# Kernel optimization log

Hardware: AMD Instinct MI355X
Metric: run time of the kernel (lower is better)

The kernel has to match this reference:

```python
import jax, jax.numpy as jnp
import numpy as np

N = 50000        # nodes
E = 1_600_000    # edges (avg degree 32)
D_IN = 128
HID = 256
D_OUT = 128      # must equal D_IN for the residual add


def setup_inputs() -> dict:
    key = jax.random.key(0)
    k0, k1, k2, k3 = jax.random.split(key, 4)
    x = jax.random.normal(k0, (N, D_IN), dtype=jnp.float32)
    edge_index = jax.random.randint(k1, (2, E), 0, N, dtype=jnp.int32)
    # GCNConv params (lin: Linear without bias in PyG, plus additive bias)
    W1 = jax.random.normal(k2, (D_IN, HID), dtype=jnp.float32) / np.sqrt(D_IN)
    b1 = jnp.zeros((HID,), jnp.float32)
    W2 = jax.random.normal(k3, (HID, D_OUT), dtype=jnp.float32) / np.sqrt(HID)
    b2 = jnp.zeros((D_OUT,), jnp.float32)
    return {"x": x, "edge_index": edge_index, "W1": W1, "b1": b1, "W2": W2, "b2": b2}


def _gcn_conv(x, src, dst, norm, W, b, n):
    # PyG GCNConv: transform, gather source features, scale by sym-norm, scatter-add to dst.
    h = x @ W                        # [n, d_out]
    msg = h[src] * norm[:, None]     # [E+n, d_out] gathered messages
    out = jax.ops.segment_sum(msg, dst, num_segments=n)
    return out + b


def reference(x, edge_index, W1, b1, W2, b2):
    n = x.shape[0]
    # add self loops (GCNConv default add_self_loops=True)
    loops = jnp.arange(n, dtype=edge_index.dtype)
    src = jnp.concatenate([edge_index[0], loops])
    dst = jnp.concatenate([edge_index[1], loops])
    # symmetric normalization D^{-1/2} (A+I) D^{-1/2}
    deg = jax.ops.segment_sum(jnp.ones_like(dst, dtype=x.dtype), dst, num_segments=n)
    dinv = jnp.where(deg > 0, jax.lax.rsqrt(deg), 0.0)
    norm = dinv[src] * dinv[dst]
    skip = x  # nn.Identity skip connection
    h = jax.nn.relu(_gcn_conv(x, src, dst, norm, W1, b1, n))
    out = _gcn_conv(h, src, dst, norm, W2, b2, n)
    # classification_layer treated as identity; original .double() cast kept in fp32
    return out + skip
```

## Files before the change

kernel.cpp:

```cpp
#include <hip/hip_runtime.h>

#define D_IN 128
#define HID 256
#define BKT_SHIFT 9
#define BKT_SIZE 512
#define CHUNK 4096
#define PAD_SLACK 4096
#define LSTR 264

typedef __attribute__((ext_vector_type(8))) short short8;
typedef __attribute__((ext_vector_type(4))) float floatx4;

static __device__ __forceinline__ unsigned short f2b(float f) {
  unsigned u = __float_as_uint(f);
  unsigned r = (u + 0x7fffu + ((u >> 16) & 1u)) >> 16;
  return (unsigned short)r;
}

static __device__ __forceinline__ void unpack8(uint4 v, float* f) {
  f[0] = __uint_as_float(v.x << 16); f[1] = __uint_as_float(v.x & 0xffff0000u);
  f[2] = __uint_as_float(v.y << 16); f[3] = __uint_as_float(v.y & 0xffff0000u);
  f[4] = __uint_as_float(v.z << 16); f[5] = __uint_as_float(v.z & 0xffff0000u);
  f[6] = __uint_as_float(v.w << 16); f[7] = __uint_as_float(v.w & 0xffff0000u);
}

static __device__ __forceinline__ void acc_fma(float* acc, uint4 v, float w) {
  float g[8];
  unpack8(v, g);
#pragma unroll
  for (int d = 0; d < 8; ++d) acc[d] = fmaf(g[d], w, acc[d]);
}


__global__ __launch_bounds__(256) void bin_hist_kernel(const int* __restrict__ dst,
                                                       int* __restrict__ bkt_cnt,
                                                       int E, int nbkt) {
  __shared__ int hist[128];
  const int tid = threadIdx.x;
  if (tid < nbkt) hist[tid] = 0;
  __syncthreads();
  const int base = blockIdx.x * CHUNK;
  const int end = min(base + CHUNK, E);
  for (int e = base + tid; e < end; e += 256)
    atomicAdd(&hist[dst[e] >> BKT_SHIFT], 1);
  __syncthreads();
  if (tid < nbkt && hist[tid] > 0) atomicAdd(&bkt_cnt[tid], hist[tid]);
}

__global__ __launch_bounds__(128) void bkt_scan_kernel(const int* __restrict__ bkt_cnt,
                                                       int* __restrict__ bkt_start,
                                                       int* __restrict__ bkt_cursor,
                                                       float* __restrict__ dinv,
                                                       int nbkt, int E, int N) {
  __shared__ int w0tot;
  const int tid = threadIdx.x;
  const int lane = tid & 63, wid = tid >> 6;
  int v = (tid < nbkt) ? bkt_cnt[tid] : 0;
  int incl = v;
#pragma unroll
  for (int off = 1; off < 64; off <<= 1) {
    int t = __shfl_up(incl, off);
    if (lane >= off) incl += t;
  }
  if (wid == 0 && lane == 63) w0tot = incl;
  __syncthreads();
  int ex = incl - v + (wid ? w0tot : 0);
  if (tid < nbkt) { bkt_start[tid] = ex; bkt_cursor[tid] = ex; }
  if (tid == 0) { bkt_start[nbkt] = E; dinv[N] = 0.f; }
}

__global__ __launch_bounds__(256) void bin_scatter_kernel(const int* __restrict__ src,
                                                          const int* __restrict__ dst,
                                                          int* __restrict__ bkt_cursor,
                                                          int* __restrict__ ebuf,
                                                          int E, int nbkt) {
  __shared__ int hist[128];
  __shared__ int bbase[128];
  const int tid = threadIdx.x;
  if (tid < nbkt) hist[tid] = 0;
  __syncthreads();
  const int base = blockIdx.x * CHUNK;
  const int end = min(base + CHUNK, E);
  for (int e = base + tid; e < end; e += 256)
    atomicAdd(&hist[dst[e] >> BKT_SHIFT], 1);
  __syncthreads();
  if (tid < nbkt) {
    int c = hist[tid];
    bbase[tid] = c > 0 ? atomicAdd(&bkt_cursor[tid], c) : 0;
    hist[tid] = 0;
  }
  __syncthreads();
  for (int e = base + tid; e < end; e += 256) {
    int d = dst[e];
    int b = d >> BKT_SHIFT;
    int off = atomicAdd(&hist[b], 1);
    ebuf[bbase[b] + off] = (src[e] << BKT_SHIFT) | (d & (BKT_SIZE - 1));
  }
}

__global__ __launch_bounds__(256) void bucket_build_kernel(const int* __restrict__ ebuf,
                                                           const int* __restrict__ bkt_start,
                                                           float* __restrict__ dinv,
                                                           int2* __restrict__ rowse,
                                                           int* __restrict__ csr,
                                                           int N, int nbkt) {
  __shared__ int hist[BKT_SIZE];
  __shared__ int srs[BKT_SIZE];
  __shared__ int wsums[4];
  const int b = blockIdx.x;
  const int tid = threadIdx.x;
  const int node0 = b << BKT_SHIFT;
  const int nloc = min(BKT_SIZE, N - node0);
  const int ebeg = bkt_start[b], eend = bkt_start[b + 1];

  hist[tid] = 0; hist[tid + 256] = 0;
  __syncthreads();
  for (int e = ebeg + tid; e < eend; e += 256)
    atomicAdd(&hist[ebuf[e] & (BKT_SIZE - 1)], 1);
  __syncthreads();

  const int h0 = hist[2 * tid], h1 = hist[2 * tid + 1];
  const int p0 = (h0 + 7) & ~7, p1 = (h1 + 7) & ~7;
  const int s = p0 + p1;
  const int lane = tid & 63, wid = tid >> 6;
  int incl = s;
#pragma unroll
  for (int off = 1; off < 64; off <<= 1) {
    int t = __shfl_up(incl, off);
    if (lane >= off) incl += t;
  }
  if (lane == 63) wsums[wid] = incl;
  __syncthreads();
  int wex = 0;
  for (int w = 0; w < wid; ++w) wex += wsums[w];
  const int ex = wex + incl - s;
  const int base = ebeg + b * PAD_SLACK;
  if (2 * tid < nloc) {
    int st = base + ex;
    dinv[node0 + 2 * tid] = rsqrtf((float)(h0 + 1));
    rowse[node0 + 2 * tid] = make_int2(st, st + p0);
    srs[2 * tid] = st;
  }
  if (2 * tid + 1 < nloc) {
    int st = base + ex + p0;
    dinv[node0 + 2 * tid + 1] = rsqrtf((float)(h1 + 1));
    rowse[node0 + 2 * tid + 1] = make_int2(st, st + p1);
    srs[2 * tid + 1] = st;
  }
  hist[2 * tid] = 0; hist[2 * tid + 1] = 0;
  __syncthreads();

  for (int e = ebeg + tid; e < eend; e += 256) {
    int u = ebuf[e];
    int l = u & (BKT_SIZE - 1);
    int pos = atomicAdd(&hist[l], 1);
    csr[srs[l] + pos] = u >> BKT_SHIFT;
  }
  __syncthreads();
  for (int l = tid; l < nloc; l += 256) {
    int deg = hist[l];
    int p = (deg + 7) & ~7;
    int s0 = srs[l];
    for (int q = s0 + deg; q < s0 + p; ++q) csr[q] = N;
  }
}


__global__ __launch_bounds__(256) void prep_kernel(const float4* __restrict__ x4,
                                                   unsigned short* __restrict__ xb, int n4,
                                                   const float* __restrict__ W1,
                                                   unsigned short* __restrict__ Wt1,
                                                   const float* __restrict__ W2,
                                                   unsigned short* __restrict__ Wt2) {
  const int nxblk = (n4 + 255) / 256;
  const int bid = blockIdx.x;
  if (bid < nxblk) {
    int i = bid * 256 + threadIdx.x;
    if (i >= n4) return;
    float4 v = x4[i];
    ushort4 o;
    o.x = f2b(v.x); o.y = f2b(v.y); o.z = f2b(v.z); o.w = f2b(v.w);
    *(ushort4*)(xb + (size_t)i * 4) = o;
  } else if (bid < nxblk + 128) {
    int e = (bid - nxblk) * 256 + threadIdx.x;
    int k = e >> 8, n = e & 255;
    Wt1[(size_t)n * D_IN + k] = f2b(W1[e]);
  } else {
    int e = (bid - nxblk - 128) * 256 + threadIdx.x;
    int k = e >> 7, n = e & 127;
    Wt2[(size_t)n * HID + k] = f2b(W2[e]);
  }
}


__global__ __launch_bounds__(256) void gemm12_kernel(const unsigned short* __restrict__ A,
                                                     const unsigned short* __restrict__ Wt1,
                                                     const float* __restrict__ b1,
                                                     const unsigned short* __restrict__ Wt2,
                                                     unsigned short* __restrict__ T, int M) {
  __shared__ unsigned short hs[64][LSTR];
  const int tid = threadIdx.x;
  const int wave = tid >> 6;
  const int lane = tid & 63;
  const int quad = lane >> 4;
  const int l16 = lane & 15;
  const int row0 = blockIdx.x * 64;

  const short8* ap[4];
#pragma unroll
  for (int g = 0; g < 4; ++g) {
    int r = row0 + g * 16 + l16;
    if (r >= M) r = M - 1;
    ap[g] = (const short8*)(A + (size_t)r * D_IN + quad * 8);
  }
  const short8* bp1 = (const short8*)(Wt1 + (size_t)(wave * 64 + l16) * D_IN + quad * 8);

  floatx4 acc1[4][4];
#pragma unroll
  for (int g = 0; g < 4; ++g)
#pragma unroll
    for (int t = 0; t < 4; ++t) acc1[g][t] = floatx4{0.f, 0.f, 0.f, 0.f};

#pragma unroll
  for (int kt = 0; kt < 4; ++kt) {
    short8 a0 = ap[0][kt * 4], a1 = ap[1][kt * 4], a2 = ap[2][kt * 4], a3 = ap[3][kt * 4];
#pragma unroll
    for (int t = 0; t < 4; ++t) {
      short8 b = bp1[kt * 4 + t * 256];
      acc1[0][t] = __builtin_amdgcn_mfma_f32_16x16x32_bf16(a0, b, acc1[0][t], 0, 0, 0);
      acc1[1][t] = __builtin_amdgcn_mfma_f32_16x16x32_bf16(a1, b, acc1[1][t], 0, 0, 0);
      acc1[2][t] = __builtin_amdgcn_mfma_f32_16x16x32_bf16(a2, b, acc1[2][t], 0, 0, 0);
      acc1[3][t] = __builtin_amdgcn_mfma_f32_16x16x32_bf16(a3, b, acc1[3][t], 0, 0, 0);
    }
  }
#pragma unroll
  for (int t = 0; t < 4; ++t) {
    const float bv = b1[wave * 64 + t * 16 + l16];
#pragma unroll
    for (int g = 0; g < 4; ++g)
#pragma unroll
      for (int r = 0; r < 4; ++r) {
        float v = acc1[g][t][r] + bv;
        v = v > 0.f ? v : 0.f;
        hs[g * 16 + quad * 4 + r][wave * 64 + t * 16 + l16] = f2b(v);
      }
  }
  __syncthreads();

  const short8* bp2 = (const short8*)(Wt2 + (size_t)(wave * 32 + l16) * HID + quad * 8);
  floatx4 acc2[4][2];
#pragma unroll
  for (int g = 0; g < 4; ++g)
#pragma unroll
    for (int t = 0; t < 2; ++t) acc2[g][t] = floatx4{0.f, 0.f, 0.f, 0.f};

#pragma unroll
  for (int kt = 0; kt < 8; ++kt) {
    short8 a0 = *(const short8*)&hs[0 * 16 + l16][kt * 32 + quad * 8];
    short8 a1 = *(const short8*)&hs[1 * 16 + l16][kt * 32 + quad * 8];
    short8 a2 = *(const short8*)&hs[2 * 16 + l16][kt * 32 + quad * 8];
    short8 a3 = *(const short8*)&hs[3 * 16 + l16][kt * 32 + quad * 8];
#pragma unroll
    for (int t = 0; t < 2; ++t) {
      short8 b = bp2[kt * 4 + t * 512];
      acc2[0][t] = __builtin_amdgcn_mfma_f32_16x16x32_bf16(a0, b, acc2[0][t], 0, 0, 0);
      acc2[1][t] = __builtin_amdgcn_mfma_f32_16x16x32_bf16(a1, b, acc2[1][t], 0, 0, 0);
      acc2[2][t] = __builtin_amdgcn_mfma_f32_16x16x32_bf16(a2, b, acc2[2][t], 0, 0, 0);
      acc2[3][t] = __builtin_amdgcn_mfma_f32_16x16x32_bf16(a3, b, acc2[3][t], 0, 0, 0);
    }
  }
  __syncthreads();

#pragma unroll
  for (int t = 0; t < 2; ++t)
#pragma unroll
    for (int g = 0; g < 4; ++g)
#pragma unroll
      for (int r = 0; r < 4; ++r)
        hs[g * 16 + quad * 4 + r][wave * 32 + t * 16 + l16] = f2b(acc2[g][t][r]);
  __syncthreads();

#pragma unroll
  for (int i = 0; i < 4; ++i) {
    const int r = i * 16 + (tid >> 4);
    const int c = (tid & 15) * 8;
    const int row = row0 + r;
    uint4 v = *(const uint4*)&hs[r][c];
    if (row < M) *(uint4*)&T[(size_t)row * D_IN + c] = v;
  }
}


template<bool SKIP_BIAS>
__global__ __launch_bounds__(256) void agg_kernel(const uint4* __restrict__ Hq,
                                                  const int2* __restrict__ rowse,
                                                  const int* __restrict__ csr,
                                                  const float* __restrict__ dinv,
                                                  const float* __restrict__ skip,
                                                  const float* __restrict__ bias,
                                                  void* __restrict__ OUT, int n) {
  const int lane = threadIdx.x & 15;
  const int node = blockIdx.x * 16 + (threadIdx.x >> 4);
  if (node >= n) return;

  const float dv = dinv[node];
  float acc[8];
  {
    uint4 sv = Hq[(size_t)node * 16 + lane];
    float f[8];
    unpack8(sv, f);
    const float ws = dv * dv;
#pragma unroll
    for (int d = 0; d < 8; ++d) acc[d] = f[d] * ws;
  }

  const int2 se = rowse[node];
  for (int j = se.x; j < se.y; j += 8) {
    int4 c0 = *(const int4*)(csr + j);
    int4 c1 = *(const int4*)(csr + j + 4);
    float w0 = dinv[c0.x] * dv, w1 = dinv[c0.y] * dv;
    float w2 = dinv[c0.z] * dv, w3 = dinv[c0.w] * dv;
    float w4 = dinv[c1.x] * dv, w5 = dinv[c1.y] * dv;
    float w6 = dinv[c1.z] * dv, w7 = dinv[c1.w] * dv;
    uint4 v0 = Hq[(size_t)c0.x * 16 + lane];
    uint4 v1 = Hq[(size_t)c0.y * 16 + lane];
    uint4 v2 = Hq[(size_t)c0.z * 16 + lane];
    uint4 v3 = Hq[(size_t)c0.w * 16 + lane];
    uint4 v4 = Hq[(size_t)c1.x * 16 + lane];
    uint4 v5 = Hq[(size_t)c1.y * 16 + lane];
    uint4 v6 = Hq[(size_t)c1.z * 16 + lane];
    uint4 v7 = Hq[(size_t)c1.w * 16 + lane];
    acc_fma(acc, v0, w0);
    acc_fma(acc, v1, w1);
    acc_fma(acc, v2, w2);
    acc_fma(acc, v3, w3);
    acc_fma(acc, v4, w4);
    acc_fma(acc, v5, w5);
    acc_fma(acc, v6, w6);
    acc_fma(acc, v7, w7);
  }

  if (SKIP_BIAS) {
    const float* sp = skip + (size_t)node * 128 + lane * 8;
    const float* bp = bias + lane * 8;
    float4 s0 = *(const float4*)sp, s1 = *(const float4*)(sp + 4);
    float4 b0 = *(const float4*)bp, b1 = *(const float4*)(bp + 4);
    float* op = (float*)OUT + (size_t)node * 128 + lane * 8;
    *(float4*)op = make_float4(acc[0] + s0.x + b0.x, acc[1] + s0.y + b0.y,
                               acc[2] + s0.z + b0.z, acc[3] + s0.w + b0.w);
    *(float4*)(op + 4) = make_float4(acc[4] + s1.x + b1.x, acc[5] + s1.y + b1.y,
                                     acc[6] + s1.z + b1.z, acc[7] + s1.w + b1.w);
  } else {
    uint4 o;
    o.x = (unsigned)f2b(acc[0]) | ((unsigned)f2b(acc[1]) << 16);
    o.y = (unsigned)f2b(acc[2]) | ((unsigned)f2b(acc[3]) << 16);
    o.z = (unsigned)f2b(acc[4]) | ((unsigned)f2b(acc[5]) << 16);
    o.w = (unsigned)f2b(acc[6]) | ((unsigned)f2b(acc[7]) << 16);
    ((uint4*)OUT)[(size_t)node * 16 + lane] = o;
  }
}


extern "C" void kernel_launch(void* const* d_in, const int* in_sizes, int n_in,
                              void* d_out, int out_size, void* d_ws, size_t ws_size,
                              hipStream_t stream) {
  const float* x  = (const float*)d_in[0];
  const int*   ei = (const int*)d_in[1];
  const float* W1 = (const float*)d_in[2];
  const float* b1 = (const float*)d_in[3];
  const float* W2 = (const float*)d_in[4];
  const float* b2 = (const float*)d_in[5];
  float* out = (float*)d_out;

  const int N = in_sizes[0] / D_IN;
  const int E = in_sizes[1] / 2;
  const int* srcA = ei;
  const int* dstA = ei + E;
  const int NBKT = (N + BKT_SIZE - 1) >> BKT_SHIFT;
  const int NCHUNK = (E + CHUNK - 1) / CHUNK;

  char* ws = (char*)d_ws;
  size_t off = 0;
  auto alloc = [&](size_t bytes) { void* p = ws + off; off = (off + bytes + 255) & ~(size_t)255; return p; };
  int*            bkt_cnt    = (int*)           alloc((size_t)NBKT * 4);
  int*            bkt_start  = (int*)           alloc((size_t)(NBKT + 1) * 4);
  int*            bkt_cursor = (int*)           alloc((size_t)NBKT * 4);
  float*          dinv       = (float*)         alloc((size_t)(N + 1) * 4);
  int2*           rowse      = (int2*)          alloc((size_t)N * 8);
  int*            ebuf       = (int*)           alloc((size_t)E * 4);
  int*            csr        = (int*)           alloc(((size_t)E + (size_t)NBKT * PAD_SLACK) * 4);
  unsigned short* xb         = (unsigned short*)alloc((size_t)(N + 1) * D_IN * 2);
  unsigned short* aggx       = (unsigned short*)alloc((size_t)N * D_IN * 2);
  unsigned short* tb         = (unsigned short*)alloc((size_t)(N + 1) * D_IN * 2);
  unsigned short* Wt1        = (unsigned short*)alloc((size_t)D_IN * HID * 2);
  unsigned short* Wt2        = (unsigned short*)alloc((size_t)D_IN * HID * 2);

  hipMemsetAsync(bkt_cnt, 0, (size_t)NBKT * 4, stream);
  bin_hist_kernel<<<NCHUNK, 256, 0, stream>>>(dstA, bkt_cnt, E, NBKT);
  bkt_scan_kernel<<<1, 128, 0, stream>>>(bkt_cnt, bkt_start, bkt_cursor, dinv, NBKT, E, N);
  bin_scatter_kernel<<<NCHUNK, 256, 0, stream>>>(srcA, dstA, bkt_cursor, ebuf, E, NBKT);
  bucket_build_kernel<<<NBKT, 256, 0, stream>>>(ebuf, bkt_start, dinv, rowse, csr, N, NBKT);

  {
    const int n4 = N * D_IN / 4;
    prep_kernel<<<(n4 + 255) / 256 + 256, 256, 0, stream>>>((const float4*)x, xb, n4,
                                                            W1, Wt1, W2, Wt2);
  }
  agg_kernel<false><<<(N + 15) / 16, 256, 0, stream>>>((const uint4*)xb, rowse, csr,
                                                       dinv, nullptr, nullptr, aggx, N);
  gemm12_kernel<<<(N + 63) / 64, 256, 0, stream>>>(aggx, Wt1, b1, Wt2, tb, N);
  agg_kernel<true><<<(N + 15) / 16, 256, 0, stream>>>((const uint4*)tb, rowse, csr,
                                                      dinv, x, b2, out, N);
}
```

Baseline: 296.4 us.

## Split bf16 feature tables into column slices mapped to XCD pairs for L2 locality

Stores the bf16 node feature tables (xb, aggx, tb) as four 32-column slices instead of row-major 128-column rows. The aggregation kernel is remapped so each block handles 64 nodes for one slice, with the slice chosen from the block index so that each pair of XCDs only touches one quarter of the gathered table. The aim is to make each XCD's L2 working set smaller for the random neighbour gathers. The cost is that the CSR and dinv traffic is read four times, once per slice. The change also adds nontemporal loads and stores for the CSR, skip and output streams, and zeroes the padding rows of each slice.

After: 373.4 us. 1.26x slower.

```diff
diff --git a/kernel.cpp b/kernel.cpp
--- a/kernel.cpp
+++ b/kernel.cpp
@@ -10,6 +10,7 @@
 
 typedef __attribute__((ext_vector_type(8))) short short8;
 typedef __attribute__((ext_vector_type(4))) float floatx4;
+typedef __attribute__((ext_vector_type(4))) int intx4;
 
 static __device__ __forceinline__ unsigned short f2b(float f) {
   unsigned u = __float_as_uint(f);
@@ -171,7 +172,11 @@
                                                    const float* __restrict__ W1,
                                                    unsigned short* __restrict__ Wt1,
                                                    const float* __restrict__ W2,
-                                                   unsigned short* __restrict__ Wt2) {
+                                                   unsigned short* __restrict__ Wt2,
+                                                   unsigned short* __restrict__ aggx,
+                                                   unsigned short* __restrict__ tb,
+                                                   int N) {
+  const int S = (N + 1) * 32;
   const int nxblk = (n4 + 255) / 256;
   const int bid = blockIdx.x;
   if (bid < nxblk) {
@@ -180,15 +185,23 @@
     float4 v = x4[i];
     ushort4 o;
     o.x = f2b(v.x); o.y = f2b(v.y); o.z = f2b(v.z); o.w = f2b(v.w);
-    *(ushort4*)(xb + (size_t)i * 4) = o;
+    const int node = i >> 5;
+    const int j = i & 31;
+    *(ushort4*)(xb + (size_t)(j >> 3) * S + (size_t)node * 32 + (j & 7) * 4) = o;
   } else if (bid < nxblk + 128) {
     int e = (bid - nxblk) * 256 + threadIdx.x;
     int k = e >> 8, n = e & 255;
     Wt1[(size_t)n * D_IN + k] = f2b(W1[e]);
-  } else {
+  } else if (bid < nxblk + 256) {
     int e = (bid - nxblk - 128) * 256 + threadIdx.x;
     int k = e >> 7, n = e & 127;
     Wt2[(size_t)n * HID + k] = f2b(W2[e]);
+  } else {
+    int t = threadIdx.x;
+    if (t >= 48) return;
+    unsigned short* buf = (t < 16) ? xb : ((t < 32) ? aggx : tb);
+    unsigned short* p = buf + (size_t)((t >> 2) & 3) * S + (size_t)N * 32 + (t & 3) * 8;
+    *(uint4*)p = make_uint4(0u, 0u, 0u, 0u);
   }
 }
 
@@ -199,6 +212,7 @@
                                                      const unsigned short* __restrict__ Wt2,
                                                      unsigned short* __restrict__ T, int M) {
   __shared__ unsigned short hs[64][LSTR];
+  const int S = (M + 1) * 32;
   const int tid = threadIdx.x;
   const int wave = tid >> 6;
   const int lane = tid & 63;
@@ -206,12 +220,12 @@
   const int l16 = lane & 15;
   const int row0 = blockIdx.x * 64;
 
-  const short8* ap[4];
+  const unsigned short* ab[4];
 #pragma unroll
   for (int g = 0; g < 4; ++g) {
     int r = row0 + g * 16 + l16;
     if (r >= M) r = M - 1;
-    ap[g] = (const short8*)(A + (size_t)r * D_IN + quad * 8);
+    ab[g] = A + (size_t)r * 32 + quad * 8;
   }
   const short8* bp1 = (const short8*)(Wt1 + (size_t)(wave * 64 + l16) * D_IN + quad * 8);
 
@@ -223,7 +237,10 @@
 
 #pragma unroll
   for (int kt = 0; kt < 4; ++kt) {
-    short8 a0 = ap[0][kt * 4], a1 = ap[1][kt * 4], a2 = ap[2][kt * 4], a3 = ap[3][kt * 4];
+    short8 a0 = *(const short8*)(ab[0] + (size_t)kt * S);
+    short8 a1 = *(const short8*)(ab[1] + (size_t)kt * S);
+    short8 a2 = *(const short8*)(ab[2] + (size_t)kt * S);
+    short8 a3 = *(const short8*)(ab[3] + (size_t)kt * S);
 #pragma unroll
     for (int t = 0; t < 4; ++t) {
       short8 b = bp1[kt * 4 + t * 256];
@@ -286,27 +303,34 @@
     const int c = (tid & 15) * 8;
     const int row = row0 + r;
     uint4 v = *(const uint4*)&hs[r][c];
-    if (row < M) *(uint4*)&T[(size_t)row * D_IN + c] = v;
+    if (row < M)
+      *(uint4*)(T + (size_t)(c >> 5) * S + (size_t)row * 32 + (c & 31)) = v;
   }
 }
 
 
 template<bool SKIP_BIAS>
-__global__ __launch_bounds__(256) void agg_kernel(const uint4* __restrict__ Hq,
+__global__ __launch_bounds__(256) void agg_kernel(const unsigned short* __restrict__ H,
                                                   const int2* __restrict__ rowse,
                                                   const int* __restrict__ csr,
                                                   const float* __restrict__ dinv,
                                                   const float* __restrict__ skip,
                                                   const float* __restrict__ bias,
                                                   void* __restrict__ OUT, int n) {
-  const int lane = threadIdx.x & 15;
-  const int node = blockIdx.x * 16 + (threadIdx.x >> 4);
+  const int bid = blockIdx.x;
+  const int xcd = bid & 7;
+  const int q = xcd >> 1;
+  const int g = ((bid >> 3) << 1) | (xcd & 1);
+  const int node = g * 64 + (threadIdx.x >> 2);
+  const int lane = threadIdx.x & 3;
   if (node >= n) return;
+  const int S = (n + 1) * 32;
+  const uint4* Hq = (const uint4*)(H + (size_t)q * S);
 
   const float dv = dinv[node];
   float acc[8];
   {
-    uint4 sv = Hq[(size_t)node * 16 + lane];
+    uint4 sv = Hq[(size_t)node * 4 + lane];
     float f[8];
     unpack8(sv, f);
     const float ws = dv * dv;
@@ -316,20 +340,20 @@
 
   const int2 se = rowse[node];
   for (int j = se.x; j < se.y; j += 8) {
-    int4 c0 = *(const int4*)(csr + j);
-    int4 c1 = *(const int4*)(csr + j + 4);
+    intx4 c0 = __builtin_nontemporal_load((const intx4*)(csr + j));
+    intx4 c1 = __builtin_nontemporal_load((const intx4*)(csr + j + 4));
     float w0 = dinv[c0.x] * dv, w1 = dinv[c0.y] * dv;
     float w2 = dinv[c0.z] * dv, w3 = dinv[c0.w] * dv;
     float w4 = dinv[c1.x] * dv, w5 = dinv[c1.y] * dv;
     float w6 = dinv[c1.z] * dv, w7 = dinv[c1.w] * dv;
-    uint4 v0 = Hq[(size_t)c0.x * 16 + lane];
-    uint4 v1 = Hq[(size_t)c0.y * 16 + lane];
-    uint4 v2 = Hq[(size_t)c0.z * 16 + lane];
-    uint4 v3 = Hq[(size_t)c0.w * 16 + lane];
-    uint4 v4 = Hq[(size_t)c1.x * 16 + lane];
-    uint4 v5 = Hq[(size_t)c1.y * 16 + lane];
-    uint4 v6 = Hq[(size_t)c1.z * 16 + lane];
-    uint4 v7 = Hq[(size_t)c1.w * 16 + lane];
+    uint4 v0 = Hq[(size_t)c0.x * 4 + lane];
+    uint4 v1 = Hq[(size_t)c0.y * 4 + lane];
+    uint4 v2 = Hq[(size_t)c0.z * 4 + lane];
+    uint4 v3 = Hq[(size_t)c0.w * 4 + lane];
+    uint4 v4 = Hq[(size_t)c1.x * 4 + lane];
+    uint4 v5 = Hq[(size_t)c1.y * 4 + lane];
+    uint4 v6 = Hq[(size_t)c1.z * 4 + lane];
+    uint4 v7 = Hq[(size_t)c1.w * 4 + lane];
     acc_fma(acc, v0, w0);
     acc_fma(acc, v1, w1);
     acc_fma(acc, v2, w2);
@@ -341,22 +365,26 @@
   }
 
   if (SKIP_BIAS) {
-    const float* sp = skip + (size_t)node * 128 + lane * 8;
-    const float* bp = bias + lane * 8;
-    float4 s0 = *(const float4*)sp, s1 = *(const float4*)(sp + 4);
-    float4 b0 = *(const float4*)bp, b1 = *(const float4*)(bp + 4);
-    float* op = (float*)OUT + (size_t)node * 128 + lane * 8;
-    *(float4*)op = make_float4(acc[0] + s0.x + b0.x, acc[1] + s0.y + b0.y,
-                               acc[2] + s0.z + b0.z, acc[3] + s0.w + b0.w);
-    *(float4*)(op + 4) = make_float4(acc[4] + s1.x + b1.x, acc[5] + s1.y + b1.y,
-                                     acc[6] + s1.z + b1.z, acc[7] + s1.w + b1.w);
+    const float* sp = skip + (size_t)node * 128 + q * 32 + lane * 8;
+    const float* bp = bias + q * 32 + lane * 8;
+    floatx4 s0 = __builtin_nontemporal_load((const floatx4*)sp);
+    floatx4 s1 = __builtin_nontemporal_load((const floatx4*)sp + 1);
+    floatx4 b0 = *(const floatx4*)bp;
+    floatx4 b1v = *(const floatx4*)(bp + 4);
+    float* op = (float*)OUT + (size_t)node * 128 + q * 32 + lane * 8;
+    floatx4 o0 = {acc[0] + s0.x + b0.x, acc[1] + s0.y + b0.y,
+                  acc[2] + s0.z + b0.z, acc[3] + s0.w + b0.w};
+    floatx4 o1 = {acc[4] + s1.x + b1v.x, acc[5] + s1.y + b1v.y,
+                  acc[6] + s1.z + b1v.z, acc[7] + s1.w + b1v.w};
+    __builtin_nontemporal_store(o0, (floatx4*)op);
+    __builtin_nontemporal_store(o1, (floatx4*)op + 1);
   } else {
     uint4 o;
     o.x = (unsigned)f2b(acc[0]) | ((unsigned)f2b(acc[1]) << 16);
     o.y = (unsigned)f2b(acc[2]) | ((unsigned)f2b(acc[3]) << 16);
     o.z = (unsigned)f2b(acc[4]) | ((unsigned)f2b(acc[5]) << 16);
     o.w = (unsigned)f2b(acc[6]) | ((unsigned)f2b(acc[7]) << 16);
-    ((uint4*)OUT)[(size_t)node * 16 + lane] = o;
+    *((uint4*)((unsigned short*)OUT + (size_t)q * S) + (size_t)node * 4 + lane) = o;
   }
 }
 
@@ -390,12 +418,12 @@
   int*            ebuf       = (int*)           alloc((size_t)E * 4);
   int*            csr        = (int*)           alloc(((size_t)E + (size_t)NBKT * PAD_SLACK) * 4);
   unsigned short* xb         = (unsigned short*)alloc((size_t)(N + 1) * D_IN * 2);
-  unsigned short* aggx       = (unsigned short*)alloc((size_t)N * D_IN * 2);
+  unsigned short* aggx       = (unsigned short*)alloc((size_t)(N + 1) * D_IN * 2);
   unsigned short* tb         = (unsigned short*)alloc((size_t)(N + 1) * D_IN * 2);
   unsigned short* Wt1        = (unsigned short*)alloc((size_t)D_IN * HID * 2);
   unsigned short* Wt2        = (unsigned short*)alloc((size_t)D_IN * HID * 2);
 
-  hipMemsetAsync(bkt_cnt, 0, (size_t)NBKT * 4, stream);
+  (void)hipMemsetAsync(bkt_cnt, 0, (size_t)NBKT * 4, stream);
   bin_hist_kernel<<<NCHUNK, 256, 0, stream>>>(dstA, bkt_cnt, E, NBKT);
   bkt_scan_kernel<<<1, 128, 0, stream>>>(bkt_cnt, bkt_start, bkt_cursor, dinv, NBKT, E, N);
   bin_scatter_kernel<<<NCHUNK, 256, 0, stream>>>(srcA, dstA, bkt_cursor, ebuf, E, NBKT);
@@ -403,12 +431,13 @@
 
   {
     const int n4 = N * D_IN / 4;
-    prep_kernel<<<(n4 + 255) / 256 + 256, 256, 0, stream>>>((const float4*)x, xb, n4,
-                                                            W1, Wt1, W2, Wt2);
-  }
-  agg_kernel<false><<<(N + 15) / 16, 256, 0, stream>>>((const uint4*)xb, rowse, csr,
-                                                       dinv, nullptr, nullptr, aggx, N);
+    prep_kernel<<<(n4 + 255) / 256 + 257, 256, 0, stream>>>((const float4*)x, xb, n4,
+                                                            W1, Wt1, W2, Wt2, aggx, tb, N);
+  }
+  int ngb = (N + 63) / 64;
+  ngb += (ngb & 1);
+  agg_kernel<false><<<4 * ngb, 256, 0, stream>>>(xb, rowse, csr, dinv,
+                                                 nullptr, nullptr, aggx, N);
   gemm12_kernel<<<(N + 63) / 64, 256, 0, stream>>>(aggx, Wt1, b1, Wt2, tb, N);
-  agg_kernel<true><<<(N + 15) / 16, 256, 0, stream>>>((const uint4*)tb, rowse, csr,
-                                                      dinv, x, b2, out, N);
-}
+  agg_kernel<true><<<4 * ngb, 256, 0, stream>>>(tb, rowse, csr, dinv, x, b2, out, N);
+}
```
